# Optimization experiments

Hardware: AMD Instinct MI355X
Metric: run time of the kernel (lower is better)

Reference implementation:

```python
import jax, jax.numpy as jnp
import numpy as np

EMBED = 1024
HEADS = 16
HEAD_DIM = EMBED // HEADS


def setup_inputs() -> dict:
    key = jax.random.key(0)
    k1, k2, k3, k4, k5 = jax.random.split(key, 5)
    B, S = 2, 2048
    scale = 1.0 / np.sqrt(EMBED)
    return {
        "input_tensor": jax.random.normal(k1, (B, S, EMBED), dtype=jnp.float32),
        "qkv_weight": jax.random.normal(k2, (3 * EMBED, EMBED), dtype=jnp.float32) * scale,
        "qkv_bias": jax.random.normal(k3, (3 * EMBED,), dtype=jnp.float32) * 0.02,
        "out_weight": jax.random.normal(k4, (EMBED, EMBED), dtype=jnp.float32) * scale,
        "out_bias": jax.random.normal(k5, (EMBED,), dtype=jnp.float32) * 0.02,
    }


def reference(input_tensor, qkv_weight, qkv_bias, out_weight, out_bias):
    B, S, D = input_tensor.shape
    # fused QKV projection: (B,S,3D)
    qkv = jnp.einsum("bsd,ed->bse", input_tensor, qkv_weight) + qkv_bias
    q, k, v = jnp.split(qkv, 3, axis=-1)
    # reshape to (B,H,S,hd)
    def to_heads(t):
        return t.reshape(B, S, HEADS, HEAD_DIM).transpose(0, 2, 1, 3)
    q, k, v = to_heads(q), to_heads(k), to_heads(v)
    scores = jnp.einsum("bhqd,bhkd->bhqk", q, k) / jnp.sqrt(jnp.float32(HEAD_DIM))
    probs = jax.nn.softmax(scores, axis=-1)  # dropout is identity in eval
    attn = jnp.einsum("bhqk,bhkd->bhqd", probs, v)
    attn = attn.transpose(0, 2, 1, 3).reshape(B, S, D)
    out = jnp.einsum("bsd,ed->bse", attn, out_weight) + out_bias
    return out
```

## Files before the change

kernel.cpp:

```cpp
#include <hip/hip_runtime.h>
#include <stdint.h>

#define EMBED 1024
#define HEADS 16
#define HD 64
#define D3 3072
#define SEQ 2048
#define MROWS 4096

typedef __attribute__((ext_vector_type(8))) short short8;
typedef __attribute__((ext_vector_type(4))) float f32x4;
typedef __attribute__((ext_vector_type(16))) float f32x16;

static __device__ __forceinline__ ushort f2bf(float f) {
    uint32_t u = __builtin_bit_cast(uint32_t, f);
    uint32_t r = (u + 0x7fffu + ((u >> 16) & 1u)) >> 16;
    return (ushort)r;
}

static __device__ __forceinline__ void glds16(const void* g, void* l) {
    __builtin_amdgcn_global_load_lds(
        (const __attribute__((address_space(1))) uint32_t*)g,
        (__attribute__((address_space(3))) uint32_t*)(uintptr_t)l,
        16, 0, 0);
}

static __device__ __forceinline__ uint32_t cvt_pk_bf16(float lo, float hi) {
    uint32_t r;
    asm("v_cvt_pk_bf16_f32 %0, %1, %2" : "=v"(r) : "v"(lo), "v"(hi));
    return r;
}

__global__ __launch_bounds__(256) void cvt_f32_bf16(const float* __restrict__ in,
                                                    ushort* __restrict__ out, int n4) {
    int i = blockIdx.x * 256 + threadIdx.x;
    if (i < n4) {
        float4 v = reinterpret_cast<const float4*>(in)[i];
        ushort4 o = { f2bf(v.x), f2bf(v.y), f2bf(v.z), f2bf(v.w) };
        reinterpret_cast<ushort4*>(out)[i] = o;
    }
}

template<int OUT_BF16>
__global__ __launch_bounds__(256) void gemm_bt_mfma(
    const ushort* __restrict__ A, const ushort* __restrict__ W,
    const float* __restrict__ bias, void* __restrict__ Cout,
    int M, int N, int K)
{
    __shared__ __align__(16) ushort As[128 * 32];
    __shared__ __align__(16) ushort Bs[128 * 32];

    const int t = threadIdx.x;
    const int lane = t & 63;
    const int w = t >> 6;
    const int wm = w >> 1, wn = w & 1;
    const int bm = blockIdx.y * 128, bn = blockIdx.x * 128;
    const int r16 = lane & 15, g = lane >> 4;

    f32x4 acc[4][4];
#pragma unroll
    for (int i = 0; i < 4; ++i)
#pragma unroll
        for (int j = 0; j < 4; ++j) acc[i][j] = (f32x4){0.f, 0.f, 0.f, 0.f};

    for (int k0 = 0; k0 < K; k0 += 32) {
#pragma unroll
        for (int p = 0; p < 2; ++p) {
            int c = t + p * 256;
            int row = c >> 2;
            int sg = (c & 3) ^ (row & 3);
            glds16(A + (size_t)(bm + row) * K + k0 + sg * 8, (char*)As + c * 16);
            glds16(W + (size_t)(bn + row) * K + k0 + sg * 8, (char*)Bs + c * 16);
        }
        __syncthreads();

        short8 af[4], bf[4];
#pragma unroll
        for (int mt = 0; mt < 4; ++mt) {
            int row = wm * 64 + mt * 16 + r16;
            int off = (g * 16) ^ ((row & 3) << 4);
            af[mt] = *reinterpret_cast<const short8*>((const char*)As + row * 64 + off);
        }
#pragma unroll
        for (int nt = 0; nt < 4; ++nt) {
            int row = wn * 64 + nt * 16 + r16;
            int off = (g * 16) ^ ((row & 3) << 4);
            bf[nt] = *reinterpret_cast<const short8*>((const char*)Bs + row * 64 + off);
        }
#pragma unroll
        for (int mt = 0; mt < 4; ++mt)
#pragma unroll
            for (int nt = 0; nt < 4; ++nt)
                acc[mt][nt] = __builtin_amdgcn_mfma_f32_16x16x32_bf16(
                    af[mt], bf[nt], acc[mt][nt], 0, 0, 0);
        __syncthreads();
    }

#pragma unroll
    for (int mt = 0; mt < 4; ++mt) {
#pragma unroll
        for (int nt = 0; nt < 4; ++nt) {
            int col = bn + wn * 64 + nt * 16 + r16;
            float bv = bias[col];
#pragma unroll
            for (int r = 0; r < 4; ++r) {
                size_t rowg = (size_t)(bm + wm * 64 + mt * 16 + g * 4 + r);
                float v = acc[mt][nt][r] + bv;
                if (OUT_BF16) ((ushort*)Cout)[rowg * N + col] = f2bf(v);
                else          ((float*)Cout)[rowg * N + col] = v;
            }
        }
    }
}

__global__ __launch_bounds__(256) void attn_mfma(
    const ushort* __restrict__ qkv, ushort* __restrict__ outb)
{
    __shared__ __align__(16) ushort lds[24576];

    const int t = threadIdx.x, lane = t & 63, w = t >> 6;
    const int qt = blockIdx.x, bh = blockIdx.y;
    const int b = bh >> 4, h = bh & 15;
    const int q31 = lane & 31, hi = lane >> 5;

    const ushort* Qb = qkv + (size_t)b * SEQ * D3 + h * HD;
    const ushort* Kb = Qb + EMBED;
    const ushort* Vb = Qb + 2 * EMBED;

    ushort* Pw = lds + 16384 + w * 2048;

    short8 qf[4];
    {
        const ushort* qrow = Qb + (size_t)(qt * 128 + w * 32 + q31) * D3 + 8 * hi;
#pragma unroll
        for (int ks = 0; ks < 4; ++ks)
            qf[ks] = *reinterpret_cast<const short8*>(qrow + ks * 16);
    }

    uint4 vv[2];
    auto stage_K = [&](int tile, ushort* dst) {
#pragma unroll
        for (int p = 0; p < 2; ++p) {
            int c = t + p * 256;
            int row = c >> 3;
            int sg = (c & 7) ^ (row & 7);
            glds16(Kb + (size_t)(tile * 64 + row) * D3 + sg * 8, (char*)dst + c * 16);
        }
    };
    auto load_V = [&](int tile) {
#pragma unroll
        for (int p = 0; p < 2; ++p) {
            int dseg = w * 2 + p;
            vv[p] = *reinterpret_cast<const uint4*>(
                Vb + (size_t)(tile * 64 + lane) * D3 + dseg * 8);
        }
    };
    auto write_V = [&](ushort* dst) {
#pragma unroll
        for (int p = 0; p < 2; ++p) {
            int dseg = w * 2 + p;
            ushort tmp[8];
            *reinterpret_cast<uint4*>(tmp) = vv[p];
#pragma unroll
            for (int j = 0; j < 8; ++j) {
                int d = dseg * 8 + j;
                int off = (lane * 2) ^ ((d & 7) << 4);
                *(ushort*)((char*)dst + d * 128 + off) = tmp[j];
            }
        }
    };

    f32x16 o[2];
#pragma unroll
    for (int db = 0; db < 2; ++db)
#pragma unroll
        for (int r = 0; r < 16; ++r) o[db][r] = 0.f;
    float m2 = -1e30f, lsum = 0.f;

    const float SC = 0.18033688011112042f;

    stage_K(0, lds);
    load_V(0);
    write_V(lds + 8192);
    __syncthreads();

    const int NT = SEQ / 64;
    for (int kt = 0; kt < NT; ++kt) {
        const int cur = kt & 1;
        ushort* Kc = lds + cur * 4096;
        ushort* Vc = lds + 8192 + cur * 4096;
        ushort* Kn = lds + (cur ^ 1) * 4096;
        ushort* Vn = lds + 8192 + (cur ^ 1) * 4096;
        const bool more = (kt + 1 < NT);

        if (more) { stage_K(kt + 1, Kn); load_V(kt + 1); }

        f32x16 s[2];
#pragma unroll
        for (int cb = 0; cb < 2; ++cb)
#pragma unroll
            for (int r = 0; r < 16; ++r) s[cb][r] = 0.f;

        __builtin_amdgcn_s_setprio(1);
#pragma unroll
        for (int cb = 0; cb < 2; ++cb) {
            int row = cb * 32 + q31;
            int swz = (row & 7) << 4;
#pragma unroll
            for (int ks = 0; ks < 4; ++ks) {
                int off = (32 * ks + 16 * hi) ^ swz;
                short8 kf = *reinterpret_cast<const short8*>((const char*)Kc + row * 128 + off);
                s[cb] = __builtin_amdgcn_mfma_f32_32x32x16_bf16(kf, qf[ks], s[cb], 0, 0, 0);
            }
        }
        __builtin_amdgcn_s_setprio(0);

        float pmax = -1e30f;
#pragma unroll
        for (int cb = 0; cb < 2; ++cb)
#pragma unroll
            for (int r = 0; r < 16; ++r) {
                s[cb][r] *= SC;
                pmax = fmaxf(pmax, s[cb][r]);
            }
        pmax = fmaxf(pmax, __shfl_xor(pmax, 32));

        if (!__all(pmax - m2 <= 8.0f)) {
            float mn = fmaxf(m2, pmax);
            float corr = exp2f(m2 - mn);
            lsum *= corr;
#pragma unroll
            for (int db = 0; db < 2; ++db)
#pragma unroll
                for (int r = 0; r < 16; ++r) o[db][r] *= corr;
            m2 = mn;
        }

        float rs = 0.f;
        int pswz = (q31 & 7) << 4;
#pragma unroll
        for (int cb = 0; cb < 2; ++cb)
#pragma unroll
            for (int r = 0; r < 16; r += 2) {
                float p0 = exp2f(s[cb][r] - m2);
                float p1 = exp2f(s[cb][r + 1] - m2);
                rs += p0 + p1;
                uint32_t pk = cvt_pk_bf16(p0, p1);
                int kc = 32 * cb + (r & 3) + 8 * (r >> 2) + 4 * hi;
                int off = (kc * 2) ^ pswz;
                *(uint32_t*)((char*)Pw + q31 * 128 + off) = pk;
            }
        rs += __shfl_xor(rs, 32);
        lsum += rs;

        asm volatile("s_waitcnt lgkmcnt(0)" ::: "memory");
        __builtin_amdgcn_sched_barrier(0);

        short8 pB[4];
#pragma unroll
        for (int ks = 0; ks < 4; ++ks) {
            int off = (32 * ks + 16 * hi) ^ pswz;
            pB[ks] = *reinterpret_cast<const short8*>((const char*)Pw + q31 * 128 + off);
        }
        __builtin_amdgcn_s_setprio(1);
#pragma unroll
        for (int db = 0; db < 2; ++db) {
            int row = db * 32 + q31;
            int swz = (row & 7) << 4;
#pragma unroll
            for (int ks = 0; ks < 4; ++ks) {
                int off = (32 * ks + 16 * hi) ^ swz;
                short8 vf = *reinterpret_cast<const short8*>((const char*)Vc + row * 128 + off);
                o[db] = __builtin_amdgcn_mfma_f32_32x32x16_bf16(vf, pB[ks], o[db], 0, 0, 0);
            }
        }
        __builtin_amdgcn_s_setprio(0);

        if (more) write_V(Vn);
        __syncthreads();
    }

    const size_t orow = (size_t)b * SEQ + qt * 128 + w * 32 + q31;
    float inv = 1.f / lsum;
#pragma unroll
    for (int db = 0; db < 2; ++db) {
#pragma unroll
        for (int m = 0; m < 4; ++m) {
            int d0 = 32 * db + 8 * m + 4 * hi;
            ushort4 ov;
            ov.x = f2bf(o[db][4 * m + 0] * inv);
            ov.y = f2bf(o[db][4 * m + 1] * inv);
            ov.z = f2bf(o[db][4 * m + 2] * inv);
            ov.w = f2bf(o[db][4 * m + 3] * inv);
            *reinterpret_cast<ushort4*>(&outb[orow * EMBED + h * HD + d0]) = ov;
        }
    }
}

extern "C" void kernel_launch(void* const* d_in, const int* in_sizes, int n_in,
                              void* d_out, int out_size, void* d_ws, size_t ws_size,
                              hipStream_t stream)
{
    const float* x    = (const float*)d_in[0];
    const float* wqkv = (const float*)d_in[1];
    const float* bqkv = (const float*)d_in[2];
    const float* wo   = (const float*)d_in[3];
    const float* bo   = (const float*)d_in[4];
    float* out = (float*)d_out;

    ushort* xb    = (ushort*)d_ws;
    ushort* wqkvb = xb + (size_t)MROWS * EMBED;
    ushort* wob   = wqkvb + (size_t)D3 * EMBED;
    ushort* qkvb  = wob + (size_t)EMBED * EMBED;
    ushort* attnb = qkvb + (size_t)MROWS * D3;

    cvt_f32_bf16<<<4096, 256, 0, stream>>>(x,    xb,    MROWS * EMBED / 4);
    cvt_f32_bf16<<<3072, 256, 0, stream>>>(wqkv, wqkvb, D3 * EMBED / 4);
    cvt_f32_bf16<<<1024, 256, 0, stream>>>(wo,   wob,   EMBED * EMBED / 4);

    gemm_bt_mfma<1><<<dim3(D3 / 128, MROWS / 128), 256, 0, stream>>>(
        xb, wqkvb, bqkv, qkvb, MROWS, D3, EMBED);

    attn_mfma<<<dim3(SEQ / 128, 2 * HEADS), 256, 0, stream>>>(qkvb, attnb);

    gemm_bt_mfma<0><<<dim3(EMBED / 128, MROWS / 128), 256, 0, stream>>>(
        attnb, wob, bo, out, MROWS, EMBED, EMBED);
}
```

Before: 224.5 us.

## Build P operand in registers via permlane32 swap instead of LDS round-trip

Replaces the LDS write/read round-trip for the softmax probability tile with v_permlane32_swap lane exchanges that rearrange the packed bf16 P values directly into the MFMA B-operand layout. The cross-half max and sum reductions also use permlane32 swap instead of shfl_xor. The scale multiply is folded into an fma inside exp2, and the lazy-rescale threshold is expressed in unscaled units. LDS per block shrinks from 48KB to 32KB, which could raise occupancy, and an lgkmcnt wait and scheduling barrier are removed. The register layout mapping must match exactly or the results will be wrong.

```diff
diff --git a/kernel.cpp b/kernel.cpp
--- a/kernel.cpp
+++ b/kernel.cpp
@@ -29,6 +29,25 @@
     uint32_t r;
     asm("v_cvt_pk_bf16_f32 %0, %1, %2" : "=v"(r) : "v"(lo), "v"(hi));
     return r;
+}
+
+static __device__ __forceinline__ void pl32swap(uint32_t& a, uint32_t& b) {
+    auto r = __builtin_amdgcn_permlane32_swap(a, b, false, false);
+    uint32_t tmp[2];
+    __builtin_memcpy(tmp, &r, 8);
+    a = tmp[0];
+    b = tmp[1];
+}
+
+static __device__ __forceinline__ float xhalf_max(float x) {
+    uint32_t a = __builtin_bit_cast(uint32_t, x), b = a;
+    pl32swap(a, b);
+    return fmaxf(__builtin_bit_cast(float, a), __builtin_bit_cast(float, b));
+}
+static __device__ __forceinline__ float xhalf_add(float x) {
+    uint32_t a = __builtin_bit_cast(uint32_t, x), b = a;
+    pl32swap(a, b);
+    return __builtin_bit_cast(float, a) + __builtin_bit_cast(float, b);
 }
 
 __global__ __launch_bounds__(256) void cvt_f32_bf16(const float* __restrict__ in,
@@ -116,7 +135,7 @@
 __global__ __launch_bounds__(256) void attn_mfma(
     const ushort* __restrict__ qkv, ushort* __restrict__ outb)
 {
-    __shared__ __align__(16) ushort lds[24576];
+    __shared__ __align__(16) ushort lds[16384];
 
     const int t = threadIdx.x, lane = t & 63, w = t >> 6;
     const int qt = blockIdx.x, bh = blockIdx.y;
@@ -126,8 +145,6 @@
     const ushort* Qb = qkv + (size_t)b * SEQ * D3 + h * HD;
     const ushort* Kb = Qb + EMBED;
     const ushort* Vb = Qb + 2 * EMBED;
-
-    ushort* Pw = lds + 16384 + w * 2048;
 
     short8 qf[4];
     {
@@ -178,6 +195,7 @@
     float m2 = -1e30f, lsum = 0.f;
 
     const float SC = 0.18033688011112042f;
+    const float THR = 44.0f;
 
     stage_K(0, lds);
     load_V(0);
@@ -219,15 +237,13 @@
 #pragma unroll
         for (int cb = 0; cb < 2; ++cb)
 #pragma unroll
-            for (int r = 0; r < 16; ++r) {
-                s[cb][r] *= SC;
-                pmax = fmaxf(pmax, s[cb][r]);
-            }
-        pmax = fmaxf(pmax, __shfl_xor(pmax, 32));
-
-        if (!__all(pmax - m2 <= 8.0f)) {
+            for (int r = 0; r < 16; r += 2)
+                pmax = fmaxf(pmax, fmaxf(s[cb][r], s[cb][r + 1]));
+        pmax = xhalf_max(pmax);
+
+        if (!__all(pmax - m2 <= THR)) {
             float mn = fmaxf(m2, pmax);
-            float corr = exp2f(m2 - mn);
+            float corr = exp2f((m2 - mn) * SC);
             lsum *= corr;
 #pragma unroll
             for (int db = 0; db < 2; ++db)
@@ -235,33 +251,34 @@
                 for (int r = 0; r < 16; ++r) o[db][r] *= corr;
             m2 = mn;
         }
-
+        const float m2s = m2 * SC;
+
+        uint32_t pk[8][2];
         float rs = 0.f;
-        int pswz = (q31 & 7) << 4;
 #pragma unroll
         for (int cb = 0; cb < 2; ++cb)
 #pragma unroll
-            for (int r = 0; r < 16; r += 2) {
-                float p0 = exp2f(s[cb][r] - m2);
-                float p1 = exp2f(s[cb][r + 1] - m2);
-                rs += p0 + p1;
-                uint32_t pk = cvt_pk_bf16(p0, p1);
-                int kc = 32 * cb + (r & 3) + 8 * (r >> 2) + 4 * hi;
-                int off = (kc * 2) ^ pswz;
-                *(uint32_t*)((char*)Pw + q31 * 128 + off) = pk;
-            }
-        rs += __shfl_xor(rs, 32);
-        lsum += rs;
-
-        asm volatile("s_waitcnt lgkmcnt(0)" ::: "memory");
-        __builtin_amdgcn_sched_barrier(0);
+            for (int rm = 0; rm < 4; ++rm)
+#pragma unroll
+                for (int wd = 0; wd < 2; ++wd) {
+                    float p0 = exp2f(fmaf(s[cb][4 * rm + 2 * wd], SC, -m2s));
+                    float p1 = exp2f(fmaf(s[cb][4 * rm + 2 * wd + 1], SC, -m2s));
+                    rs += p0 + p1;
+                    pk[4 * cb + rm][wd] = cvt_pk_bf16(p0, p1);
+                }
+        lsum += xhalf_add(rs);
 
         short8 pB[4];
 #pragma unroll
         for (int ks = 0; ks < 4; ++ks) {
-            int off = (32 * ks + 16 * hi) ^ pswz;
-            pB[ks] = *reinterpret_cast<const short8*>((const char*)Pw + q31 * 128 + off);
-        }
+            uint32_t a0 = pk[2 * ks][0], b0 = pk[2 * ks + 1][0];
+            uint32_t a1 = pk[2 * ks][1], b1 = pk[2 * ks + 1][1];
+            pl32swap(a0, b0);
+            pl32swap(a1, b1);
+            uint4 fr = { a0, a1, b0, b1 };
+            pB[ks] = __builtin_bit_cast(short8, fr);
+        }
+
         __builtin_amdgcn_s_setprio(1);
 #pragma unroll
         for (int db = 0; db < 2; ++db) {
```

New measurement: 225.8 us. About the same (+0.6%).
